# Kernel optimization log

Hardware: AMD Instinct MI355X
Metric: run time of the kernel (lower is better)

Reference implementation:

```python
import jax, jax.numpy as jnp
import numpy as np

K, N, MEM_D = 512, 4096, 64


def setup_inputs() -> dict:
    key = jax.random.key(0)
    k1, k2, k3, k4 = jax.random.split(key, 4)
    # event counts per location/time (torch code uses raw observations; rand in [0,1) keeps log-lik finite)
    obs = jax.random.uniform(k1, (K, N), jnp.float32)
    extobs = jax.random.normal(k2, (K, N), jnp.float32)
    beta = jnp.asarray(2.0, jnp.float32)  # torch.Tensor([2]) scalar rate parameter
    alpha = jax.random.uniform(k3, (K, K), jnp.float32, 0.0, 0.01)
    gamma = jax.random.uniform(k4, (K, MEM_D), jnp.float32, 0.0, 0.01)
    return {"obs": obs, "extobs": extobs, "beta": beta, "alpha": alpha, "gamma": gamma}


def reference(obs, extobs, beta, alpha, gamma):
    Kk, Nn = obs.shape
    d = gamma.shape[1]
    # mu is derived from obs exactly as in __init__ (not a trainable parameter)
    mu = obs.mean(axis=1) / 10.0 + 0.01  # [K]

    t = jnp.arange(Nn)
    diff = t[:, None] - t[None, :]  # [N, N], diff[t, j] = t - j
    # strict lower-triangular exponential decay kernel: D[t, j] = beta * exp(-(t-j)*beta) for j < t
    # clamp diff before exp so masked entries never produce inf (keeps vjp NaN-free)
    safe = jnp.maximum(diff, 1).astype(jnp.float32)
    Dmat = jnp.where(diff > 0, beta * jnp.exp(-safe * beta), 0.0)  # [N, N]

    # lam1[k, t] = sum_{k'} alpha[k, k'] * sum_{j < t} obs[k', j] * beta * exp(-(t-j)*beta)
    lam1 = alpha @ (obs @ Dmat.T)  # [K, N]

    # lam2[k, t] = sum_i extobs[k, t-d+i] * gamma[k, i]  (only when t >= d, else 0)
    # depthwise 1D cross-correlation with left zero-padding of d, then mask t < d
    x = extobs[None]            # [1, K, N]
    w = gamma[:, None, :]       # [K, 1, d]
    lam2 = jax.lax.conv_general_dilated(
        x, w, window_strides=(1,), padding=[(d, 0)],
        dimension_numbers=("NCH", "OIH", "NCH"), feature_group_count=Kk,
    )[0, :, :Nn]                # [K, N]
    lam2 = jnp.where(t[None, :] >= d, lam2, 0.0)

    lams = jax.nn.softplus(mu[:, None] + lam1 + lam2)  # [K, N]
    loglik = (obs * jnp.log(lams) - lams).sum()
    return (loglik, lams)
```

## Files before the change

### kernel.cpp

```cpp
#include <hip/hip_runtime.h>
#include <math.h>

#define KDIM 512
#define NDIM 4096
#define MEMD 64
#define WTAPS 16

#define GBM 64
#define GBN 64
#define GBK 64

typedef short bf16x8 __attribute__((ext_vector_type(8)));
typedef float f32x4 __attribute__((ext_vector_type(4)));

#define GLOAD_LDS16(g, l) __builtin_amdgcn_global_load_lds( \
    (const __attribute__((address_space(1))) unsigned int*)(g), \
    (__attribute__((address_space(3))) unsigned int*)(l), 16, 0, 0)

__device__ __forceinline__ void bsplit(float a, ushort& hi, ushort& lo) {
    uint u = __float_as_uint(a);
    uint h = (u + 0x7FFFu + ((u >> 16) & 1u)) >> 16;
    hi = (ushort)h;
    float hf = __uint_as_float(h << 16);
    float r = a - hf;
    uint u2 = __float_as_uint(r);
    lo = (ushort)((u2 + 0x7FFFu + ((u2 >> 16) & 1u)) >> 16);
}

__device__ __forceinline__ float block_reduce_256(float v, float* sbuf) {
    #pragma unroll
    for (int off = 32; off > 0; off >>= 1) v += __shfl_down(v, off, 64);
    int lane = threadIdx.x & 63, wid = threadIdx.x >> 6;
    if (lane == 0) sbuf[wid] = v;
    __syncthreads();
    float tot = sbuf[0] + sbuf[1] + sbuf[2] + sbuf[3];
    __syncthreads();
    return tot;
}

__device__ __forceinline__ double block_reduce_256d(double v, double* dbuf) {
    #pragma unroll
    for (int off = 32; off > 0; off >>= 1) v += __shfl_down(v, off, 64);
    int lane = threadIdx.x & 63, wid = threadIdx.x >> 6;
    if (lane == 0) dbuf[wid] = v;
    __syncthreads();
    double tot = dbuf[0] + dbuf[1] + dbuf[2] + dbuf[3];
    __syncthreads();
    return tot;
}

__global__ __launch_bounds__(256) void conv_kernel(
    const float* __restrict__ B, const float* __restrict__ A,
    ushort* __restrict__ Bthi, ushort* __restrict__ Btlo,
    ushort* __restrict__ Ahi, ushort* __restrict__ Alo,
    unsigned int* __restrict__ cnt) {
    __shared__ float s[32][33];
    int b = blockIdx.x, tid = threadIdx.x;
    if (b < 2048) {
        int n0 = (b & 127) * 32, k0 = (b >> 7) * 32;
        int r = tid >> 5, c = tid & 31;
        #pragma unroll
        for (int i = 0; i < 4; ++i)
            s[r + i * 8][c] = B[(size_t)(k0 + r + i * 8) * NDIM + n0 + c];
        __syncthreads();
        int rr = tid >> 4, cc = (tid & 15) * 2;
        #pragma unroll
        for (int i = 0; i < 2; ++i) {
            int n = rr + i * 16;
            float a0 = s[cc][n], a1 = s[cc + 1][n];
            ushort h0, l0, h1, l1;
            bsplit(a0, h0, l0); bsplit(a1, h1, l1);
            size_t o = (size_t)(n0 + n) * KDIM + k0 + cc;
            *(ushort2*)&Bthi[o] = make_ushort2(h0, h1);
            *(ushort2*)&Btlo[o] = make_ushort2(l0, l1);
        }
    } else {
        int ab = b - 2048;
        if (ab == 0 && tid == 0) *cnt = 0u;
        int g = ab * 256 + tid;
        const float4* src = (const float4*)A;
        #pragma unroll
        for (int i = 0; i < 2; ++i) {
            float4 v = src[g * 2 + i];
            ushort4 h, l;
            bsplit(v.x, h.x, l.x); bsplit(v.y, h.y, l.y);
            bsplit(v.z, h.z, l.z); bsplit(v.w, h.w, l.w);
            *(ushort4*)&Ahi[(size_t)g * 8 + i * 4] = h;
            *(ushort4*)&Alo[(size_t)g * 8 + i * 4] = l;
        }
    }
}

__global__ __launch_bounds__(256) void mfma_gemm(
    const ushort* __restrict__ Ahi, const ushort* __restrict__ Alo,
    const ushort* __restrict__ Bthi, const ushort* __restrict__ Btlo,
    float* __restrict__ C) {
    __shared__ __align__(16) ushort Asm[2][GBM * GBK];
    __shared__ __align__(16) ushort Bsm[2][GBN * GBK];
    int tid = threadIdx.x;
    int m0 = blockIdx.y * GBM, n0 = blockIdx.x * GBN;
    int l = tid & 63, w = tid >> 6;
    int wm = w >> 1, wn = w & 1;
    int lr = l & 15, lk = l >> 4;

    f32x4 acc[2][2];
    #pragma unroll
    for (int i = 0; i < 2; ++i)
        #pragma unroll
        for (int j = 0; j < 2; ++j) acc[i][j] = (f32x4){0.f, 0.f, 0.f, 0.f};

    for (int c0 = 0; c0 < KDIM; c0 += GBK) {
        #pragma unroll
        for (int i = 0; i < 4; ++i) {
            int c = tid + i * 256;
            int plane = c >> 9, q = c & 511;
            int row = q >> 3, kc = (q & 7) ^ (row & 7);
            const ushort* sa = (plane ? Alo : Ahi) + (size_t)(m0 + row) * KDIM + c0 + kc * 8;
            GLOAD_LDS16(sa, (char*)&Asm[0][0] + c * 16);
            const ushort* sb = (plane ? Btlo : Bthi) + (size_t)(n0 + row) * KDIM + c0 + kc * 8;
            GLOAD_LDS16(sb, (char*)&Bsm[0][0] + c * 16);
        }
        __syncthreads();
        bf16x8 ah[2][2], al[2][2], bh[2][2], bl[2][2];
        #pragma unroll
        for (int mf = 0; mf < 2; ++mf)
            #pragma unroll
            for (int s = 0; s < 2; ++s) {
                int ra = wm * 32 + mf * 16 + lr;
                int offa = ra * 128 + (((s * 64) + lk * 16) ^ ((ra & 7) << 4));
                ah[mf][s] = *(const bf16x8*)((const char*)&Asm[0][0] + offa);
                al[mf][s] = *(const bf16x8*)((const char*)&Asm[1][0] + offa);
                int rb = wn * 32 + mf * 16 + lr;
                int offb = rb * 128 + (((s * 64) + lk * 16) ^ ((rb & 7) << 4));
                bh[mf][s] = *(const bf16x8*)((const char*)&Bsm[0][0] + offb);
                bl[mf][s] = *(const bf16x8*)((const char*)&Bsm[1][0] + offb);
            }
        #pragma unroll
        for (int s = 0; s < 2; ++s)
            #pragma unroll
            for (int mf = 0; mf < 2; ++mf)
                #pragma unroll
                for (int nf = 0; nf < 2; ++nf) {
                    acc[mf][nf] = __builtin_amdgcn_mfma_f32_16x16x32_bf16(ah[mf][s], bh[nf][s], acc[mf][nf], 0, 0, 0);
                    acc[mf][nf] = __builtin_amdgcn_mfma_f32_16x16x32_bf16(ah[mf][s], bl[nf][s], acc[mf][nf], 0, 0, 0);
                    acc[mf][nf] = __builtin_amdgcn_mfma_f32_16x16x32_bf16(al[mf][s], bh[nf][s], acc[mf][nf], 0, 0, 0);
                }
        __syncthreads();
    }
    #pragma unroll
    for (int mf = 0; mf < 2; ++mf)
        #pragma unroll
        for (int nf = 0; nf < 2; ++nf)
            #pragma unroll
            for (int j = 0; j < 4; ++j) {
                int rm = m0 + wm * 32 + mf * 16 + lk * 4 + j;
                int cn = n0 + wn * 32 + nf * 16 + lr;
                C[(size_t)rm * NDIM + cn] = acc[mf][nf][j];
            }
}

__device__ __forceinline__ int chunk_off(int cch) {
    return ((cch & ~7) | ((cch ^ (cch >> 3)) & 7)) * 16;
}
__device__ __forceinline__ float4 lds_chunk(const float* buf, int cch) {
    return *(const float4*)((const char*)buf + chunk_off(cch));
}
__device__ __forceinline__ void lds_chunk_store(float* buf, int cch, float4 v) {
    *(float4*)((char*)buf + chunk_off(cch)) = v;
}

__global__ __launch_bounds__(256) void final_kernel(
    const float* __restrict__ T, const float* __restrict__ obs,
    const float* __restrict__ extobs, const float* __restrict__ gamma,
    const float* __restrict__ beta_p,
    float* __restrict__ lams_out, double* __restrict__ partials,
    unsigned int* __restrict__ cnt, float* __restrict__ loglik_out) {
    __shared__ float Trow[NDIM];
    __shared__ float Erow[NDIM];
    __shared__ float Orow[NDIM];
    __shared__ float Grow[MEMD];
    __shared__ float sbuf[4];
    __shared__ double dbuf[4];
    __shared__ unsigned int flagS;

    int k = blockIdx.x, tid = threadIdx.x;
    float beta = *beta_p;

    const float4* t4 = (const float4*)(T + (size_t)k * NDIM);
    const float4* e4 = (const float4*)(extobs + (size_t)k * NDIM);
    const float4* o4 = (const float4*)(obs + (size_t)k * NDIM);

    float osum = 0.f;
    #pragma unroll
    for (int i = 0; i < 4; ++i) {
        int c = tid + i * 256;
        lds_chunk_store(Trow, c, t4[c]);
        lds_chunk_store(Erow, c, e4[c]);
        float4 o = o4[c];
        lds_chunk_store(Orow, c, o);
        osum += (o.x + o.y) + (o.z + o.w);
    }
    if (tid < MEMD) Grow[tid] = gamma[(size_t)k * MEMD + tid];

    float wtap[WTAPS];
    #pragma unroll
    for (int m = 0; m < WTAPS; ++m) wtap[m] = beta * expf(-beta * (float)(m + 1));

    float mu;
    {
        float tot = block_reduce_256(osum, sbuf);
        mu = tot / (float)NDIM / 10.0f + 0.01f;
    }

    int t0 = tid * 16;

    float l1[16];
    #pragma unroll
    for (int j = 0; j < 16; ++j) l1[j] = 0.f;
    {
        float win[32];
        int cb = tid * 4 - 4;
        #pragma unroll
        for (int c = 0; c < 8; ++c) {
            int idx = cb + c;
            float4 x = (idx >= 0) ? lds_chunk(Trow, idx) : make_float4(0.f, 0.f, 0.f, 0.f);
            *(float4*)&win[c * 4] = x;
        }
        #pragma unroll
        for (int m = 1; m <= WTAPS; ++m) {
            float wm = wtap[m - 1];
            #pragma unroll
            for (int j = 0; j < 16; ++j) l1[j] = fmaf(wm, win[16 + j - m], l1[j]);
        }
    }

    float l2[16];
    #pragma unroll
    for (int j = 0; j < 16; ++j) l2[j] = 0.f;
    if (tid >= 4) {
        #pragma unroll
        for (int c4 = 0; c4 < 4; ++c4) {
            float win[32];
            int cb = tid * 4 - 16 + c4 * 4;
            #pragma unroll
            for (int c = 0; c < 8; ++c)
                *(float4*)&win[c * 4] = lds_chunk(Erow, cb + c);
            #pragma unroll
            for (int i = 0; i < 16; ++i) {
                float g = Grow[c4 * 16 + i];
                #pragma unroll
                for (int j = 0; j < 16; ++j) l2[j] = fmaf(g, win[i + j], l2[j]);
            }
        }
    }

    float* lrp = lams_out + (size_t)k * NDIM;
    double part = 0.0;
    #pragma unroll
    for (int i = 0; i < 4; ++i) {
        float4 o = lds_chunk(Orow, tid * 4 + i);
        float oo[4] = {o.x, o.y, o.z, o.w};
        f32x4 sv;
        #pragma unroll
        for (int q = 0; q < 4; ++q) {
            int j = i * 4 + q;
            float x = mu + l1[j] + l2[j];
            float sp = fmaxf(x, 0.f) + log1pf(expf(-fabsf(x)));
            sv[q] = sp;
            part += (double)(oo[q] * logf(sp) - sp);
        }
        *(f32x4*)&lrp[t0 + i * 4] = sv;
    }
    double dtot = block_reduce_256d(part, dbuf);
    if (tid == 0) {
        partials[k] = dtot;
        __threadfence();
        unsigned int old = atomicAdd(cnt, 1u);
        flagS = (old == (unsigned int)(KDIM - 1)) ? 1u : 0u;
    }
    __syncthreads();
    if (flagS) {
        __threadfence();
        double v = 0.0;
        for (int j = tid; j < KDIM; j += 256) v += partials[j];
        double tot = block_reduce_256d(v, dbuf);
        if (tid == 0) loglik_out[0] = (float)tot;
    }
}

extern "C" void kernel_launch(void* const* d_in, const int* in_sizes, int n_in,
                              void* d_out, int out_size, void* d_ws, size_t ws_size,
                              hipStream_t stream) {
    const float* obs    = (const float*)d_in[0];
    const float* extobs = (const float*)d_in[1];
    const float* beta   = (const float*)d_in[2];
    const float* alpha  = (const float*)d_in[3];
    const float* gamma  = (const float*)d_in[4];
    float* out = (float*)d_out;

    char* ws = (char*)d_ws;
    float*  T        = (float*)(ws);
    ushort* Bthi     = (ushort*)(ws + (8u << 20));
    ushort* Btlo     = (ushort*)(ws + (12u << 20));
    ushort* Ahi      = (ushort*)(ws + (16u << 20));
    ushort* Alo      = (ushort*)(ws + (16u << 20) + (512u << 10));
    double* partials = (double*)(ws + (17u << 20));
    unsigned int* cnt = (unsigned int*)(ws + (17u << 20) + 4096);

    conv_kernel<<<2048 + 128, 256, 0, stream>>>(obs, alpha, Bthi, Btlo, Ahi, Alo, cnt);
    mfma_gemm<<<dim3(NDIM / GBN, KDIM / GBM), 256, 0, stream>>>(Ahi, Alo, Bthi, Btlo, T);
    final_kernel<<<KDIM, 256, 0, stream>>>(T, obs, extobs, gamma, beta,
                                           out + 1, partials, cnt, out);
}
```

Before: 121.1 us.

## Split final kernel into per-row segments and precompute mu in prep kernel

```diff
diff --git a/kernel.cpp b/kernel.cpp
--- a/kernel.cpp
+++ b/kernel.cpp
@@ -5,6 +5,9 @@
 #define NDIM 4096
 #define MEMD 64
 #define WTAPS 16
+#define SEG 1024
+#define NSEG (NDIM / SEG)
+#define NPART (KDIM * NSEG)
 
 #define GBM 64
 #define GBN 64
@@ -53,7 +56,7 @@
     const float* __restrict__ B, const float* __restrict__ A,
     ushort* __restrict__ Bthi, ushort* __restrict__ Btlo,
     ushort* __restrict__ Ahi, ushort* __restrict__ Alo,
-    unsigned int* __restrict__ cnt) {
+    unsigned int* __restrict__ cnt, float* __restrict__ mu) {
     __shared__ float s[32][33];
     int b = blockIdx.x, tid = threadIdx.x;
     if (b < 2048) {
@@ -74,9 +77,9 @@
             *(ushort2*)&Bthi[o] = make_ushort2(h0, h1);
             *(ushort2*)&Btlo[o] = make_ushort2(l0, l1);
         }
-    } else {
+    } else if (b < 2176) {
         int ab = b - 2048;
-        if (ab == 0 && tid == 0) *cnt = 0u;
+        if (ab == 0 && tid == 0) atomicExch(cnt, 0u);
         int g = ab * 256 + tid;
         const float4* src = (const float4*)A;
         #pragma unroll
@@ -88,6 +91,13 @@
             *(ushort4*)&Ahi[(size_t)g * 8 + i * 4] = h;
             *(ushort4*)&Alo[(size_t)g * 8 + i * 4] = l;
         }
+    } else {
+        int k = b - 2176;
+        const float* row = B + (size_t)k * NDIM;
+        float ss = 0.f;
+        for (int j = tid; j < NDIM; j += 256) ss += row[j];
+        float tot = block_reduce_256(ss, &s[0][0]);
+        if (tid == 0) mu[k] = tot / (float)NDIM / 10.0f + 0.01f;
     }
 }
 
@@ -159,130 +169,104 @@
             }
 }
 
-__device__ __forceinline__ int chunk_off(int cch) {
-    return ((cch & ~7) | ((cch ^ (cch >> 3)) & 7)) * 16;
-}
-__device__ __forceinline__ float4 lds_chunk(const float* buf, int cch) {
-    return *(const float4*)((const char*)buf + chunk_off(cch));
-}
-__device__ __forceinline__ void lds_chunk_store(float* buf, int cch, float4 v) {
-    *(float4*)((char*)buf + chunk_off(cch)) = v;
-}
-
-__global__ __launch_bounds__(256) void final_kernel(
+__global__ __launch_bounds__(256, 6) void final_kernel(
     const float* __restrict__ T, const float* __restrict__ obs,
     const float* __restrict__ extobs, const float* __restrict__ gamma,
-    const float* __restrict__ beta_p,
+    const float* __restrict__ beta_p, const float* __restrict__ mu,
     float* __restrict__ lams_out, double* __restrict__ partials,
     unsigned int* __restrict__ cnt, float* __restrict__ loglik_out) {
-    __shared__ float Trow[NDIM];
-    __shared__ float Erow[NDIM];
-    __shared__ float Orow[NDIM];
-    __shared__ float Grow[MEMD];
-    __shared__ float sbuf[4];
+    __shared__ float Ts[SEG + 16];
+    __shared__ float Es[SEG + 64];
+    __shared__ float Os[SEG];
+    __shared__ float Gs[MEMD];
+    __shared__ float Wt[WTAPS];
     __shared__ double dbuf[4];
     __shared__ unsigned int flagS;
 
-    int k = blockIdx.x, tid = threadIdx.x;
+    int b = blockIdx.x, tid = threadIdx.x;
+    int k = b >> 2, s = b & 3;
     float beta = *beta_p;
-
-    const float4* t4 = (const float4*)(T + (size_t)k * NDIM);
-    const float4* e4 = (const float4*)(extobs + (size_t)k * NDIM);
-    const float4* o4 = (const float4*)(obs + (size_t)k * NDIM);
-
-    float osum = 0.f;
-    #pragma unroll
-    for (int i = 0; i < 4; ++i) {
-        int c = tid + i * 256;
-        lds_chunk_store(Trow, c, t4[c]);
-        lds_chunk_store(Erow, c, e4[c]);
-        float4 o = o4[c];
-        lds_chunk_store(Orow, c, o);
-        osum += (o.x + o.y) + (o.z + o.w);
-    }
-    if (tid < MEMD) Grow[tid] = gamma[(size_t)k * MEMD + tid];
-
-    float wtap[WTAPS];
-    #pragma unroll
-    for (int m = 0; m < WTAPS; ++m) wtap[m] = beta * expf(-beta * (float)(m + 1));
-
-    float mu;
+    float muk = mu[k];
+
+    const float4* gT = (const float4*)(T + (size_t)k * NDIM);
+    const float4* gE = (const float4*)(extobs + (size_t)k * NDIM);
+    const float4* gO = (const float4*)(obs + (size_t)k * NDIM);
+    float4 z = make_float4(0.f, 0.f, 0.f, 0.f);
+
     {
-        float tot = block_reduce_256(osum, sbuf);
-        mu = tot / (float)NDIM / 10.0f + 0.01f;
-    }
-
-    int t0 = tid * 16;
-
-    float l1[16];
-    #pragma unroll
-    for (int j = 0; j < 16; ++j) l1[j] = 0.f;
-    {
-        float win[32];
-        int cb = tid * 4 - 4;
-        #pragma unroll
-        for (int c = 0; c < 8; ++c) {
-            int idx = cb + c;
-            float4 x = (idx >= 0) ? lds_chunk(Trow, idx) : make_float4(0.f, 0.f, 0.f, 0.f);
-            *(float4*)&win[c * 4] = x;
-        }
-        #pragma unroll
-        for (int m = 1; m <= WTAPS; ++m) {
-            float wm = wtap[m - 1];
+        #pragma unroll
+        for (int i = tid; i < 260; i += 256) {
+            int gi = s * 256 - 4 + i;
+            ((float4*)Ts)[i] = (gi >= 0) ? gT[gi] : z;
+        }
+        #pragma unroll
+        for (int i = tid; i < 272; i += 256) {
+            int gi = s * 256 - 16 + i;
+            ((float4*)Es)[i] = (gi >= 0) ? gE[gi] : z;
+        }
+        ((float4*)Os)[tid] = gO[s * 256 + tid];
+        if (tid < MEMD) Gs[tid] = gamma[(size_t)k * MEMD + tid];
+        if (tid >= 64 && tid < 64 + WTAPS) {
+            int m = tid - 63;
+            Wt[m - 1] = beta * expf(-beta * (float)m);
+        }
+    }
+    __syncthreads();
+
+    int t_loc = tid * 4;
+    int t = s * SEG + t_loc;
+    float win[20];
+    float l1[4] = {0.f, 0.f, 0.f, 0.f};
+    float l2[4] = {0.f, 0.f, 0.f, 0.f};
+
+    #pragma unroll
+    for (int c = 0; c < 5; ++c) *(float4*)&win[c * 4] = *(const float4*)&Ts[t_loc + c * 4];
+    #pragma unroll
+    for (int m = 1; m <= WTAPS; ++m) {
+        float wm = Wt[m - 1];
+        #pragma unroll
+        for (int j = 0; j < 4; ++j) l1[j] = fmaf(wm, win[16 + j - m], l1[j]);
+    }
+
+    #pragma unroll
+    for (int c4 = 0; c4 < 4; ++c4) {
+        #pragma unroll
+        for (int c = 0; c < 5; ++c)
+            *(float4*)&win[c * 4] = *(const float4*)&Es[t_loc + c4 * 16 + c * 4];
+        #pragma unroll
+        for (int i = 0; i < 16; ++i) {
+            float g = Gs[c4 * 16 + i];
             #pragma unroll
-            for (int j = 0; j < 16; ++j) l1[j] = fmaf(wm, win[16 + j - m], l1[j]);
-        }
-    }
-
-    float l2[16];
-    #pragma unroll
-    for (int j = 0; j < 16; ++j) l2[j] = 0.f;
-    if (tid >= 4) {
-        #pragma unroll
-        for (int c4 = 0; c4 < 4; ++c4) {
-            float win[32];
-            int cb = tid * 4 - 16 + c4 * 4;
-            #pragma unroll
-            for (int c = 0; c < 8; ++c)
-                *(float4*)&win[c * 4] = lds_chunk(Erow, cb + c);
-            #pragma unroll
-            for (int i = 0; i < 16; ++i) {
-                float g = Grow[c4 * 16 + i];
-                #pragma unroll
-                for (int j = 0; j < 16; ++j) l2[j] = fmaf(g, win[i + j], l2[j]);
-            }
-        }
-    }
-
-    float* lrp = lams_out + (size_t)k * NDIM;
+            for (int j = 0; j < 4; ++j) l2[j] = fmaf(g, win[i + j], l2[j]);
+        }
+    }
+    if (t < MEMD) { l2[0] = 0.f; l2[1] = 0.f; l2[2] = 0.f; l2[3] = 0.f; }
+
+    float4 o = ((const float4*)Os)[tid];
+    float oo[4] = {o.x, o.y, o.z, o.w};
     double part = 0.0;
-    #pragma unroll
-    for (int i = 0; i < 4; ++i) {
-        float4 o = lds_chunk(Orow, tid * 4 + i);
-        float oo[4] = {o.x, o.y, o.z, o.w};
-        f32x4 sv;
-        #pragma unroll
-        for (int q = 0; q < 4; ++q) {
-            int j = i * 4 + q;
-            float x = mu + l1[j] + l2[j];
-            float sp = fmaxf(x, 0.f) + log1pf(expf(-fabsf(x)));
-            sv[q] = sp;
-            part += (double)(oo[q] * logf(sp) - sp);
-        }
-        *(f32x4*)&lrp[t0 + i * 4] = sv;
-    }
+    f32x4 sv;
+    #pragma unroll
+    for (int j = 0; j < 4; ++j) {
+        float x = muk + l1[j] + l2[j];
+        float sp = fmaxf(x, 0.f) + log1pf(expf(-fabsf(x)));
+        sv[j] = sp;
+        part += (double)(oo[j] * logf(sp) - sp);
+    }
+    *(f32x4*)&lams_out[(size_t)k * NDIM + t] = sv;
+
     double dtot = block_reduce_256d(part, dbuf);
     if (tid == 0) {
-        partials[k] = dtot;
+        partials[b] = dtot;
         __threadfence();
         unsigned int old = atomicAdd(cnt, 1u);
-        flagS = (old == (unsigned int)(KDIM - 1)) ? 1u : 0u;
+        flagS = (old == (unsigned int)(NPART - 1)) ? 1u : 0u;
     }
     __syncthreads();
     if (flagS) {
         __threadfence();
         double v = 0.0;
-        for (int j = tid; j < KDIM; j += 256) v += partials[j];
+        for (int j = tid; j < NPART; j += 256) v += partials[j];
         double tot = block_reduce_256d(v, dbuf);
         if (tid == 0) loglik_out[0] = (float)tot;
     }
@@ -305,10 +289,12 @@
     ushort* Ahi      = (ushort*)(ws + (16u << 20));
     ushort* Alo      = (ushort*)(ws + (16u << 20) + (512u << 10));
     double* partials = (double*)(ws + (17u << 20));
-    unsigned int* cnt = (unsigned int*)(ws + (17u << 20) + 4096);
-
-    conv_kernel<<<2048 + 128, 256, 0, stream>>>(obs, alpha, Bthi, Btlo, Ahi, Alo, cnt);
+    unsigned int* cnt = (unsigned int*)(ws + (17u << 20) + (16u << 10));
+    float* mu        = (float*)(ws + (17u << 20) + (16u << 10) + 256);
+
+    conv_kernel<<<2048 + 128 + 512, 256, 0, stream>>>(obs, alpha, Bthi, Btlo,
+                                                      Ahi, Alo, cnt, mu);
     mfma_gemm<<<dim3(NDIM / GBN, KDIM / GBM), 256, 0, stream>>>(Ahi, Alo, Bthi, Btlo, T);
-    final_kernel<<<KDIM, 256, 0, stream>>>(T, obs, extobs, gamma, beta,
-                                           out + 1, partials, cnt, out);
-}
+    final_kernel<<<NPART, 256, 0, stream>>>(T, obs, extobs, gamma, beta, mu,
+                                            out + 1, partials, cnt, out);
+}
```

New measurement: 161.4 us. 33.2% more time.
